# Performance work log

Hardware: AMD Instinct MI355X
Metric: run time of the kernel (lower is better)

Reference implementation:

```python
import jax, jax.numpy as jnp
import numpy as np

B, T, I, H, HORIZON = 64, 512, 256, 1024, 24


def _lstm_layer(x, Wih, Whh, bih, bhh):
    """PyTorch-convention LSTM layer. x: [B,T,I_l] -> outputs [B,T,H].
    Gate order along 4H axis: i, f, g, o."""
    b = x.shape[0]
    h_dim = Whh.shape[1]
    # Precompute input contribution for all timesteps: [B,T,4H]
    xg = jnp.einsum('bti,gi->btg', x, Wih) + bih + bhh

    def step(carry, xg_t):
        h, c = carry
        gates = xg_t + h @ Whh.T  # [B,4H]
        i_g, f_g, g_g, o_g = jnp.split(gates, 4, axis=-1)
        c = jax.nn.sigmoid(f_g) * c + jax.nn.sigmoid(i_g) * jnp.tanh(g_g)
        h = jax.nn.sigmoid(o_g) * jnp.tanh(c)
        return (h, c), h

    h0 = jnp.zeros((b, h_dim), x.dtype)
    (_, _), hs = jax.lax.scan(step, (h0, h0), jnp.swapaxes(xg, 0, 1))
    return jnp.swapaxes(hs, 0, 1)  # [B,T,H]


def setup_inputs() -> dict:
    key = jax.random.key(0)
    ks = jax.random.split(key, 11)
    s_i = 1.0 / np.sqrt(H)  # PyTorch-style uniform-ish scale, use scaled normal
    return {
        'x': jax.random.normal(ks[0], (B, T, I), jnp.float32),
        'W_ih0': jax.random.normal(ks[1], (4 * H, I), jnp.float32) * s_i,
        'W_hh0': jax.random.normal(ks[2], (4 * H, H), jnp.float32) * s_i,
        'b_ih0': jax.random.normal(ks[3], (4 * H,), jnp.float32) * s_i,
        'b_hh0': jax.random.normal(ks[4], (4 * H,), jnp.float32) * s_i,
        'W_ih1': jax.random.normal(ks[5], (4 * H, H), jnp.float32) * s_i,
        'W_hh1': jax.random.normal(ks[6], (4 * H, H), jnp.float32) * s_i,
        'b_ih1': jax.random.normal(ks[7], (4 * H,), jnp.float32) * s_i,
        'b_hh1': jax.random.normal(ks[8], (4 * H,), jnp.float32) * s_i,
        'W_head': jax.random.normal(ks[9], (HORIZON, H), jnp.float32) * s_i,
        'b_head': jax.random.normal(ks[10], (HORIZON,), jnp.float32) * s_i,
    }


def reference(x, W_ih0, W_hh0, b_ih0, b_hh0, W_ih1, W_hh1, b_ih1, b_hh1, W_head, b_head):
    h1 = _lstm_layer(x, W_ih0, W_hh0, b_ih0, b_hh0)   # [B,T,H]
    h2 = _lstm_layer(h1, W_ih1, W_hh1, b_ih1, b_hh1)  # [B,T,H]
    last = h2[:, -1, :]                                # [B,H]
    return last @ W_head.T + b_head                    # [B,HORIZON]
```

## Files before the change

kernel.cpp:

```cpp
#include <hip/hip_runtime.h>


typedef _Float16 h8 __attribute__((ext_vector_type(8)));
typedef float    f4 __attribute__((ext_vector_type(4)));
typedef unsigned long long u64;

#define WS_W0P   0
#define WS_W1P   10485760
#define WS_H0Q   27262976
#define WS_H2Q   27787264
#define WS_SYNC  28049408
#define WS_XPK   28057600
#define WS_XPK_END 44834816ULL

static __device__ __forceinline__ float sigm(float v) { return 1.f / (1.f + __expf(-v)); }
static __device__ __forceinline__ float tanh_fast(float v) {
  const float e = __expf(2.f * v);
  return 1.f - 2.f / (e + 1.f);
}
static __device__ __forceinline__ h8 vload16(const _Float16* p) {
  return *(const volatile h8*)p;
}
static __device__ __forceinline__ void vstore16(_Float16* p, h8 v) {
  *(volatile h8*)p = v;
}

__global__ void prep_kernel(const float* __restrict__ x,
                            const float* __restrict__ Wih0, const float* __restrict__ Whh0,
                            const float* __restrict__ Wih1, const float* __restrict__ Whh1,
                            _Float16* __restrict__ W0p, _Float16* __restrict__ W1p,
                            _Float16* __restrict__ xpk,
                            unsigned* __restrict__ hz, unsigned* __restrict__ sync_ws)
{
  const long tid0 = (long)blockIdx.x * blockDim.x + threadIdx.x;
  const long np   = (long)gridDim.x * blockDim.x;

  for (long e = tid0; e < 5242880; e += np) {
    const int j = e & 7, quad = (e >> 3) & 3, l15 = (e >> 5) & 15, nt = (e >> 9) & 7;
    const int r = (int)(e >> 12);
    const int c = r % 40, cs = r / 40;
    const int col = nt * 16 + l15;
    const int row = (col >> 5) * 1024 + cs * 32 + (col & 31);
    const int k = c * 32 + quad * 8 + j;
    const float v = (k < 256) ? Wih0[(long)row * 256 + k] : Whh0[(long)row * 1024 + k - 256];
    W0p[e] = (_Float16)v;
  }
  for (long e = tid0; e < 8388608; e += np) {
    const int j = e & 7, quad = (e >> 3) & 3, l15 = (e >> 5) & 15, nt = (e >> 9) & 7;
    const int r = (int)(e >> 12);
    const int c = r & 63, cs = r >> 6;
    const int col = nt * 16 + l15;
    const int row = (col >> 5) * 1024 + cs * 32 + (col & 31);
    const int k = c * 32 + quad * 8 + j;
    const float v = (k < 1024) ? Wih1[(long)row * 1024 + k] : Whh1[(long)row * 1024 + k - 1024];
    W1p[e] = (_Float16)v;
  }
  if (xpk) {
    for (long e = tid0; e < 8388608; e += np) {
      const int k32 = e & 31, b16 = (e >> 5) & 15, bg = (e >> 9) & 3;
      const int c = (e >> 11) & 7;
      const int t = (int)(e >> 14);
      const int b = bg * 16 + b16, k = c * 32 + k32;
      xpk[e] = (_Float16)x[(long)b * 131072 + (long)t * 256 + k];
    }
  }
  for (long e = tid0; e < 196608; e += np) hz[e] = 0u;
  if (tid0 < 2048) sync_ws[tid0] = 0u;
}

template<bool XP>
__launch_bounds__(512, 1)
__global__ void lstm_kernel(const float* __restrict__ x, const _Float16* __restrict__ xpk,
                            const float* __restrict__ bih0, const float* __restrict__ bhh0,
                            const float* __restrict__ bih1, const float* __restrict__ bhh1,
                            const _Float16* __restrict__ W0p, const _Float16* __restrict__ W1p,
                            _Float16* __restrict__ h0q, _Float16* __restrict__ h2q,
                            unsigned* __restrict__ sy)
{
  extern __shared__ float gb[];
  __shared__ float cst[512];
  __shared__ float biasl[128];
  __shared__ _Float16 htmp[32 * 18];

  const int tid = threadIdx.x, wg = blockIdx.x;
  const int xcd = wg & 7, jdec = wg >> 3;
  const int lay = jdec & 1, jj = jdec >> 1;
  const int bg = jj & 3, csl = jj >> 2;
  const int cs = xcd * 4 + csl;
  const int lidx = bg * 32 + cs;
  const int g = lidx >> 3;
  const int lane = tid & 63, kg = tid >> 6;
  const int l15 = lane & 15, quad = lane >> 4;
  const int boff = l15 * 32 + quad * 8;
  const int aoff = bg * 512 + l15 * 32 + quad * 8;

  const _Float16* Wp = lay ? (W1p + (long)cs * 262144) : (W0p + (long)cs * 163840);

  if (tid < 128) {
    const int row = (tid >> 5) * 1024 + cs * 32 + (tid & 31);
    biasl[tid] = lay ? (bih1[row] + bhh1[row]) : (bih0[row] + bhh0[row]);
  }
  cst[tid] = 0.f;
  __syncthreads();

  unsigned* const own  = sy + lay * 1024;
  unsigned* const myF  = own + 512 + g * 16;
  unsigned* const otF  = sy + (1 - lay) * 1024 + 512 + g * 16;

  auto spin_ge = [&](const unsigned* p, int target) {
    while ((int)__hip_atomic_load(p, __ATOMIC_RELAXED, __HIP_MEMORY_SCOPE_AGENT) < target)
      __builtin_amdgcn_s_sleep(2);
  };
  auto arrive = [&](unsigned e) {
    const unsigned prev = __hip_atomic_fetch_add(own + g * 16, 1u,
                            __ATOMIC_RELAXED, __HIP_MEMORY_SCOPE_AGENT);
    if (prev == 8u * e - 1u) {
      const unsigned p2 = __hip_atomic_fetch_add(own + 384, 1u,
                            __ATOMIC_RELAXED, __HIP_MEMORY_SCOPE_AGENT);
      if (p2 == 16u * e - 1u) {
#pragma unroll
        for (int i = 0; i < 16; ++i)
          __hip_atomic_store(own + 512 + i * 16, e,
                             __ATOMIC_RELAXED, __HIP_MEMORY_SCOPE_AGENT);
      }
    }
  };

  auto dump = [&](const f4* acc) {
#pragma unroll
    for (int nt = 0; nt < 8; ++nt)
      *(f4*)&gb[(kg * 128 + nt * 16 + l15) * 20 + quad * 4] = acc[nt];
  };

  auto pointwise_publish = [&](_Float16* wr) {
    __syncthreads();
    {
      const int b16 = tid & 15, hh = tid >> 4;
      float gv[4];
#pragma unroll
      for (int gt = 0; gt < 4; ++gt) {
        float s = biasl[gt * 32 + hh];
#pragma unroll
        for (int k = 0; k < 8; ++k) s += gb[(k * 128 + gt * 32 + hh) * 20 + b16];
        gv[gt] = s;
      }
      const float si = sigm(gv[0]), sf = sigm(gv[1]);
      const float tg = tanh_fast(gv[2]), so = sigm(gv[3]);
      const float cn = sf * cst[tid] + si * tg;
      cst[tid] = cn;
      htmp[hh * 18 + b16] = (_Float16)(so * tanh_fast(cn));
    }
    __syncthreads();
    if (tid < 64) {
      const int b16 = tid & 15, q = tid >> 4;
      union { h8 v; _Float16 e[8]; } r;
#pragma unroll
      for (int i = 0; i < 8; ++i) r.e[i] = htmp[(q * 8 + i) * 18 + b16];
      vstore16(wr + (cs * 4 + bg) * 512 + b16 * 32 + q * 8, r.v);
    }
    __syncthreads();
  };

  if (lay == 0) {
    const int c0 = kg * 5;
    for (int n = 0; n < 512; ++n) {
      if (tid == 0) { spin_ge(myF, n); spin_ge(otF, n - 3); }
      __syncthreads();
      const _Float16* h0prev = h0q + ((n - 1) & 3) * 65536;
      const _Float16* xs = XP ? (xpk + (long)n * 16384) : nullptr;

      f4 acc[8] = {};
      h8 Ab[2]; h8 Bb[2][8];
      auto loadAB = [&](int i, int sl) {
        const int c = c0 + i;
        const _Float16* bp = Wp + (long)c * 4096 + boff;
#pragma unroll
        for (int nt = 0; nt < 8; ++nt) Bb[sl][nt] = *(const h8*)(bp + nt * 512);
        if (c < 8) {
          if (XP) Ab[sl] = *(const h8*)(xs + c * 2048 + aoff);
          else {
            const float* q = x + (long)(bg * 16 + l15) * 131072 + (long)n * 256 + c * 32 + quad * 8;
            const f4 v0 = *(const f4*)q;
            const f4 v1 = *(const f4*)(q + 4);
            h8 t;
            t[0]=(_Float16)v0[0]; t[1]=(_Float16)v0[1]; t[2]=(_Float16)v0[2]; t[3]=(_Float16)v0[3];
            t[4]=(_Float16)v1[0]; t[5]=(_Float16)v1[1]; t[6]=(_Float16)v1[2]; t[7]=(_Float16)v1[3];
            Ab[sl] = t;
          }
        } else {
          Ab[sl] = vload16(h0prev + (c - 8) * 2048 + aoff);
        }
      };
      loadAB(0, 0);
#pragma unroll
      for (int i = 0; i < 5; ++i) {
        if (i + 1 < 5) loadAB(i + 1, (i + 1) & 1);
        const h8 A = Ab[i & 1];
#pragma unroll
        for (int nt = 0; nt < 8; ++nt)
          acc[nt] = __builtin_amdgcn_mfma_f32_16x16x32_f16(A, Bb[i & 1][nt], acc[nt], 0, 0, 0);
      }
      dump(acc);
      pointwise_publish(h0q + (n & 3) * 65536);
      if (tid == 0) arrive((unsigned)n + 1u);
    }
  } else {
    const int c0 = kg * 4;
    for (int n = 0; n < 512; ++n) {
      if (tid == 0) spin_ge(otF, n + 1);
      __syncthreads();
      const _Float16* h0cur = h0q + (n & 3) * 65536;
      const _Float16* h2prev = h2q + ((n - 1) & 1) * 65536;

      f4 acc[8] = {};
      h8 Ab[2]; h8 Bb[2][8];
      auto loadAB = [&](const _Float16* hbase, int cw, int cloc, int sl) {
        const _Float16* bp = Wp + (long)cw * 4096 + boff;
#pragma unroll
        for (int nt = 0; nt < 8; ++nt) Bb[sl][nt] = *(const h8*)(bp + nt * 512);
        Ab[sl] = vload16(hbase + cloc * 2048 + aoff);
      };
      loadAB(h0cur, c0, c0, 0);
#pragma unroll
      for (int i = 0; i < 4; ++i) {
        if (i + 1 < 4) loadAB(h0cur, c0 + i + 1, c0 + i + 1, (i + 1) & 1);
        const h8 A = Ab[i & 1];
#pragma unroll
        for (int nt = 0; nt < 8; ++nt)
          acc[nt] = __builtin_amdgcn_mfma_f32_16x16x32_f16(A, Bb[i & 1][nt], acc[nt], 0, 0, 0);
      }
      if (tid == 0) spin_ge(myF, n);
      __syncthreads();
      loadAB(h2prev, 32 + c0, c0, 0);
#pragma unroll
      for (int i = 0; i < 4; ++i) {
        if (i + 1 < 4) loadAB(h2prev, 32 + c0 + i + 1, c0 + i + 1, (i + 1) & 1);
        const h8 A = Ab[i & 1];
#pragma unroll
        for (int nt = 0; nt < 8; ++nt)
          acc[nt] = __builtin_amdgcn_mfma_f32_16x16x32_f16(A, Bb[i & 1][nt], acc[nt], 0, 0, 0);
      }
      dump(acc);
      pointwise_publish(h2q + (n & 1) * 65536);
      if (tid == 0) arrive((unsigned)n + 1u);
    }
  }
}

__global__ void head_kernel(const _Float16* __restrict__ h2s, const float* __restrict__ Wh,
                            const float* __restrict__ bh, float* __restrict__ out)
{
  const int blk = blockIdx.x;
  const int b = blk / 24, j = blk % 24;
  const int lane = threadIdx.x;
  float sum = 0.f;
#pragma unroll
  for (int k0 = 0; k0 < 1024; k0 += 64) {
    const int hid = k0 + lane;
    const float hv = (float)h2s[((hid >> 5) * 4 + (b >> 4)) * 512 + (b & 15) * 32 + (hid & 31)];
    sum += hv * Wh[(long)j * 1024 + hid];
  }
#pragma unroll
  for (int off = 32; off > 0; off >>= 1)
    sum += __shfl_down(sum, off, 64);
  if (lane == 0) out[b * 24 + j] = sum + bh[j];
}

extern "C" void kernel_launch(void* const* d_in, const int* in_sizes, int n_in,
                              void* d_out, int out_size, void* d_ws, size_t ws_size,
                              hipStream_t stream)
{
  const float* x    = (const float*)d_in[0];
  const float* Wih0 = (const float*)d_in[1];
  const float* Whh0 = (const float*)d_in[2];
  const float* bih0 = (const float*)d_in[3];
  const float* bhh0 = (const float*)d_in[4];
  const float* Wih1 = (const float*)d_in[5];
  const float* Whh1 = (const float*)d_in[6];
  const float* bih1 = (const float*)d_in[7];
  const float* bhh1 = (const float*)d_in[8];
  const float* Whd  = (const float*)d_in[9];
  const float* bhd  = (const float*)d_in[10];

  char* ws = (char*)d_ws;
  _Float16* W0p     = (_Float16*)(ws + WS_W0P);
  _Float16* W1p     = (_Float16*)(ws + WS_W1P);
  _Float16* h0q     = (_Float16*)(ws + WS_H0Q);
  _Float16* h2q     = (_Float16*)(ws + WS_H2Q);
  unsigned* sync_ws = (unsigned*)(ws + WS_SYNC);
  float* out = (float*)d_out;

  const bool use_xpk = (ws_size >= WS_XPK_END);
  _Float16* xpk = use_xpk ? (_Float16*)(ws + WS_XPK) : nullptr;

  prep_kernel<<<dim3(2048), dim3(256), 0, stream>>>(
      x, Wih0, Whh0, Wih1, Whh1, W0p, W1p, xpk,
      (unsigned*)(ws + WS_H0Q), sync_ws);

  if (use_xpk)
    lstm_kernel<true><<<dim3(256), dim3(512), 81920, stream>>>(
        x, xpk, bih0, bhh0, bih1, bhh1, W0p, W1p, h0q, h2q, sync_ws);
  else
    lstm_kernel<false><<<dim3(256), dim3(512), 81920, stream>>>(
        x, nullptr, bih0, bhh0, bih1, bhh1, W0p, W1p, h0q, h2q, sync_ws);

  head_kernel<<<dim3(64 * 24), dim3(64), 0, stream>>>(
      h2q + 65536, Whd, bhd, out);
}
```

Before: 4.843 ms.

## Use flat per-layer counters, deeper h0 ring, and prefetch weights before spin-wait

Replaces the hierarchical group/global arrive barrier with one atomic counter per layer that all 128 workgroups increment, and waits on counts of 128*n. The h0 ring buffer grows from 4 to 8 slots, so layer 0 can run up to 7 steps ahead of layer 1. Weight fragments are now loaded into registers before the spin-wait so their latency overlaps the synchronisation. Layer 1 does its h2-recurrent half first, before waiting on layer 0. The LDS gate-dump stride drops from 20 to 18 floats using 2-wide stores. The trade-offs are heavy contention on a single atomic address per layer, higher register pressure from holding 32 preloaded B vectors, and possible LDS bank conflicts.

```diff
diff --git a/kernel.cpp b/kernel.cpp
--- a/kernel.cpp
+++ b/kernel.cpp
@@ -3,15 +3,15 @@
 
 typedef _Float16 h8 __attribute__((ext_vector_type(8)));
 typedef float    f4 __attribute__((ext_vector_type(4)));
-typedef unsigned long long u64;
+typedef float    f2 __attribute__((ext_vector_type(2)));
 
 #define WS_W0P   0
 #define WS_W1P   10485760
 #define WS_H0Q   27262976
-#define WS_H2Q   27787264
-#define WS_SYNC  28049408
-#define WS_XPK   28057600
-#define WS_XPK_END 44834816ULL
+#define WS_H2Q   28311552
+#define WS_SYNC  28573696
+#define WS_XPK   28581888
+#define WS_XPK_END 45359104ULL
 
 static __device__ __forceinline__ float sigm(float v) { return 1.f / (1.f + __expf(-v)); }
 static __device__ __forceinline__ float tanh_fast(float v) {
@@ -64,7 +64,7 @@
       xpk[e] = (_Float16)x[(long)b * 131072 + (long)t * 256 + k];
     }
   }
-  for (long e = tid0; e < 196608; e += np) hz[e] = 0u;
+  for (long e = tid0; e < 327680; e += np) hz[e] = 0u;
   if (tid0 < 2048) sync_ws[tid0] = 0u;
 }
 
@@ -87,8 +87,6 @@
   const int lay = jdec & 1, jj = jdec >> 1;
   const int bg = jj & 3, csl = jj >> 2;
   const int cs = xcd * 4 + csl;
-  const int lidx = bg * 32 + cs;
-  const int g = lidx >> 3;
   const int lane = tid & 63, kg = tid >> 6;
   const int l15 = lane & 15, quad = lane >> 4;
   const int boff = l15 * 32 + quad * 8;
@@ -103,35 +101,37 @@
   cst[tid] = 0.f;
   __syncthreads();
 
-  unsigned* const own  = sy + lay * 1024;
-  unsigned* const myF  = own + 512 + g * 16;
-  unsigned* const otF  = sy + (1 - lay) * 1024 + 512 + g * 16;
+  unsigned* const L0done = sy;
+  unsigned* const L1done = sy + 16;
 
   auto spin_ge = [&](const unsigned* p, int target) {
     while ((int)__hip_atomic_load(p, __ATOMIC_RELAXED, __HIP_MEMORY_SCOPE_AGENT) < target)
       __builtin_amdgcn_s_sleep(2);
   };
-  auto arrive = [&](unsigned e) {
-    const unsigned prev = __hip_atomic_fetch_add(own + g * 16, 1u,
-                            __ATOMIC_RELAXED, __HIP_MEMORY_SCOPE_AGENT);
-    if (prev == 8u * e - 1u) {
-      const unsigned p2 = __hip_atomic_fetch_add(own + 384, 1u,
-                            __ATOMIC_RELAXED, __HIP_MEMORY_SCOPE_AGENT);
-      if (p2 == 16u * e - 1u) {
-#pragma unroll
-        for (int i = 0; i < 16; ++i)
-          __hip_atomic_store(own + 512 + i * 16, e,
-                             __ATOMIC_RELAXED, __HIP_MEMORY_SCOPE_AGENT);
-      }
-    }
-  };
-
+  auto arrive = [&](unsigned* ctr) {
+    __hip_atomic_fetch_add(ctr, 1u, __ATOMIC_RELAXED, __HIP_MEMORY_SCOPE_AGENT);
+  };
+
+  auto loadB = [&](h8* Bv, int c) {
+    const _Float16* bp = Wp + (long)c * 4096 + boff;
+#pragma unroll
+    for (int nt = 0; nt < 8; ++nt) Bv[nt] = *(const h8*)(bp + nt * 512);
+  };
+  auto consume = [&](const h8 A, const h8* Bv, f4* acc) {
+#pragma unroll
+    for (int nt = 0; nt < 8; ++nt)
+      acc[nt] = __builtin_amdgcn_mfma_f32_16x16x32_f16(A, Bv[nt], acc[nt], 0, 0, 0);
+  };
   auto dump = [&](const f4* acc) {
 #pragma unroll
-    for (int nt = 0; nt < 8; ++nt)
-      *(f4*)&gb[(kg * 128 + nt * 16 + l15) * 20 + quad * 4] = acc[nt];
-  };
-
+    for (int nt = 0; nt < 8; ++nt) {
+      const int base = (kg * 128 + nt * 16 + l15) * 18 + quad * 4;
+      f2 lo = {acc[nt][0], acc[nt][1]};
+      f2 hi = {acc[nt][2], acc[nt][3]};
+      *(f2*)&gb[base]     = lo;
+      *(f2*)&gb[base + 2] = hi;
+    }
+  };
   auto pointwise_publish = [&](_Float16* wr) {
     __syncthreads();
     {
@@ -141,7 +141,7 @@
       for (int gt = 0; gt < 4; ++gt) {
         float s = biasl[gt * 32 + hh];
 #pragma unroll
-        for (int k = 0; k < 8; ++k) s += gb[(k * 128 + gt * 32 + hh) * 20 + b16];
+        for (int k = 0; k < 8; ++k) s += gb[(k * 128 + gt * 32 + hh) * 18 + b16];
         gv[gt] = s;
       }
       const float si = sigm(gv[0]), sf = sigm(gv[1]);
@@ -164,20 +164,21 @@
   if (lay == 0) {
     const int c0 = kg * 5;
     for (int n = 0; n < 512; ++n) {
-      if (tid == 0) { spin_ge(myF, n); spin_ge(otF, n - 3); }
+      h8 Bq[4][8];
+#pragma unroll
+      for (int i = 0; i < 4; ++i) loadB(Bq[i], c0 + i);
+      __builtin_amdgcn_sched_barrier(0);
+      if (tid == 0) { spin_ge(L0done, 128 * n); spin_ge(L1done, 128 * (n - 7)); }
       __syncthreads();
-      const _Float16* h0prev = h0q + ((n - 1) & 3) * 65536;
+
+      const _Float16* h0prev = h0q + ((n - 1) & 7) * 65536;
       const _Float16* xs = XP ? (xpk + (long)n * 16384) : nullptr;
-
-      f4 acc[8] = {};
-      h8 Ab[2]; h8 Bb[2][8];
-      auto loadAB = [&](int i, int sl) {
+      h8 Ah[5];
+#pragma unroll
+      for (int i = 0; i < 5; ++i) {
         const int c = c0 + i;
-        const _Float16* bp = Wp + (long)c * 4096 + boff;
-#pragma unroll
-        for (int nt = 0; nt < 8; ++nt) Bb[sl][nt] = *(const h8*)(bp + nt * 512);
         if (c < 8) {
-          if (XP) Ab[sl] = *(const h8*)(xs + c * 2048 + aoff);
+          if (XP) Ah[i] = *(const h8*)(xs + c * 2048 + aoff);
           else {
             const float* q = x + (long)(bg * 16 + l15) * 131072 + (long)n * 256 + c * 32 + quad * 8;
             const f4 v0 = *(const f4*)q;
@@ -185,64 +186,55 @@
             h8 t;
             t[0]=(_Float16)v0[0]; t[1]=(_Float16)v0[1]; t[2]=(_Float16)v0[2]; t[3]=(_Float16)v0[3];
             t[4]=(_Float16)v1[0]; t[5]=(_Float16)v1[1]; t[6]=(_Float16)v1[2]; t[7]=(_Float16)v1[3];
-            Ab[sl] = t;
+            Ah[i] = t;
           }
         } else {
-          Ab[sl] = vload16(h0prev + (c - 8) * 2048 + aoff);
+          Ah[i] = vload16(h0prev + (c - 8) * 2048 + aoff);
         }
-      };
-      loadAB(0, 0);
-#pragma unroll
-      for (int i = 0; i < 5; ++i) {
-        if (i + 1 < 5) loadAB(i + 1, (i + 1) & 1);
-        const h8 A = Ab[i & 1];
-#pragma unroll
-        for (int nt = 0; nt < 8; ++nt)
-          acc[nt] = __builtin_amdgcn_mfma_f32_16x16x32_f16(A, Bb[i & 1][nt], acc[nt], 0, 0, 0);
       }
+      f4 acc[8] = {};
+      consume(Ah[0], Bq[0], acc);
+      loadB(Bq[0], c0 + 4);
+      consume(Ah[1], Bq[1], acc);
+      consume(Ah[2], Bq[2], acc);
+      consume(Ah[3], Bq[3], acc);
+      consume(Ah[4], Bq[0], acc);
       dump(acc);
-      pointwise_publish(h0q + (n & 3) * 65536);
-      if (tid == 0) arrive((unsigned)n + 1u);
+      pointwise_publish(h0q + (n & 7) * 65536);
+      if (tid == 0) arrive(L0done);
     }
   } else {
     const int c0 = kg * 4;
     for (int n = 0; n < 512; ++n) {
-      if (tid == 0) spin_ge(otF, n + 1);
+      h8 Bq[4][8];
+#pragma unroll
+      for (int i = 0; i < 4; ++i) loadB(Bq[i], 32 + c0 + i);
+      __builtin_amdgcn_sched_barrier(0);
+      if (tid == 0) spin_ge(L1done, 128 * n);
       __syncthreads();
-      const _Float16* h0cur = h0q + (n & 3) * 65536;
-      const _Float16* h2prev = h2q + ((n - 1) & 1) * 65536;
-
+
+      const _Float16* h2p = h2q + ((n - 1) & 1) * 65536;
+      h8 Ah[4];
+#pragma unroll
+      for (int i = 0; i < 4; ++i) Ah[i] = vload16(h2p + (c0 + i) * 2048 + aoff);
       f4 acc[8] = {};
-      h8 Ab[2]; h8 Bb[2][8];
-      auto loadAB = [&](const _Float16* hbase, int cw, int cloc, int sl) {
-        const _Float16* bp = Wp + (long)cw * 4096 + boff;
-#pragma unroll
-        for (int nt = 0; nt < 8; ++nt) Bb[sl][nt] = *(const h8*)(bp + nt * 512);
-        Ab[sl] = vload16(hbase + cloc * 2048 + aoff);
-      };
-      loadAB(h0cur, c0, c0, 0);
 #pragma unroll
       for (int i = 0; i < 4; ++i) {
-        if (i + 1 < 4) loadAB(h0cur, c0 + i + 1, c0 + i + 1, (i + 1) & 1);
-        const h8 A = Ab[i & 1];
-#pragma unroll
-        for (int nt = 0; nt < 8; ++nt)
-          acc[nt] = __builtin_amdgcn_mfma_f32_16x16x32_f16(A, Bb[i & 1][nt], acc[nt], 0, 0, 0);
+        consume(Ah[i], Bq[i], acc);
+        loadB(Bq[i], c0 + i);
       }
-      if (tid == 0) spin_ge(myF, n);
+
+      if (tid == 0) spin_ge(L0done, 128 * (n + 1));
       __syncthreads();
-      loadAB(h2prev, 32 + c0, c0, 0);
-#pragma unroll
-      for (int i = 0; i < 4; ++i) {
-        if (i + 1 < 4) loadAB(h2prev, 32 + c0 + i + 1, c0 + i + 1, (i + 1) & 1);
-        const h8 A = Ab[i & 1];
-#pragma unroll
-        for (int nt = 0; nt < 8; ++nt)
-          acc[nt] = __builtin_amdgcn_mfma_f32_16x16x32_f16(A, Bb[i & 1][nt], acc[nt], 0, 0, 0);
-      }
+      const _Float16* h0c = h0q + (n & 7) * 65536;
+#pragma unroll
+      for (int i = 0; i < 4; ++i) Ah[i] = vload16(h0c + (c0 + i) * 2048 + aoff);
+#pragma unroll
+      for (int i = 0; i < 4; ++i) consume(Ah[i], Bq[i], acc);
+
       dump(acc);
       pointwise_publish(h2q + (n & 1) * 65536);
-      if (tid == 0) arrive((unsigned)n + 1u);
+      if (tid == 0) arrive(L1done);
     }
   }
 }
```

Result: slower. 6.898 ms (+42.4%).
